# Optimization experiments

Hardware: AMD Instinct MI355X
Metric: run time of the kernel (lower is better)

The kernel has to match this reference:

```python
import jax, jax.numpy as jnp
import numpy as np

B, L, D = 4, 8192, 256          # batch, seq length, embedding dim
H, HD = 8, 32                   # heads, head dim (H*HD == D)
WN, P, S = 9, 4, 1              # window size, padding, stride
EPS = 1e-5


def _layer_norm(x, g, b):
    m = jnp.mean(x, axis=-1, keepdims=True)
    v = jnp.mean(jnp.square(x - m), axis=-1, keepdims=True)
    return (x - m) / jnp.sqrt(v + EPS) * g + b


def setup_inputs() -> dict:
    key = jax.random.key(0)
    ks = jax.random.split(key, 8)
    sc = 0.05
    return {
        "x": jax.random.normal(ks[0], (B, L, D), jnp.float32),
        "W_q": jax.random.normal(ks[1], (D, D), jnp.float32) * sc,
        "W_k": jax.random.normal(ks[2], (D, D), jnp.float32) * sc,
        "W_v": jax.random.normal(ks[3], (D, D), jnp.float32) * sc,
        "W_o": jax.random.normal(ks[4], (D, D), jnp.float32) * sc,
        "pos": jax.random.normal(ks[5], (WN, D), jnp.float32) * sc,
        "W_out": jax.random.normal(ks[6], (D, D), jnp.float32) * sc,
        "b_out": jnp.zeros((D,), jnp.float32),
        "g1": jnp.ones((D,), jnp.float32),
        "b1": jnp.zeros((D,), jnp.float32),
        "g2": jnp.ones((D,), jnp.float32),
        "b2": jnp.zeros((D,), jnp.float32),
    }


def reference(x, W_q, W_k, W_v, W_o, pos, W_out, b_out, g1, b1, g2, b2):
    # input_dim == embedding_dim -> no input projection
    padded = jnp.pad(x, ((0, 0), (P, P), (0, 0)))
    nw = (L + 2 * P - WN) // S + 1  # == L for S=1, WN=2P+1
    idx = jnp.arange(nw)[:, None] * S + jnp.arange(WN)[None, :]  # [nw, WN]
    win = padded[:, idx] + pos  # [B, nw, WN, D]

    def proj(w):  # [B, nw, WN, H, HD]
        return jnp.einsum('bnwd,de->bnwe', win, w).reshape(B, nw, WN, H, HD)

    q, k, v = proj(W_q), proj(W_k), proj(W_v)
    scale = 1.0 / (HD ** 0.5)
    scores = jnp.einsum('bnqhd,bnkhd->bnhqk', q, k) * scale  # [B,nw,H,WN,WN]
    attn = jax.nn.softmax(scores, axis=-1)
    # context, summed over query positions within each window (use_mean=False)
    ctx = jnp.einsum('bnhqk,bnkhd->bnhd', attn, v).reshape(B, nw, D)
    skip = x[:, ::S]  # [B, nw, D]
    attn_res = _layer_norm(skip + ctx @ W_o, g1, b1)
    out = _layer_norm(attn_res @ W_out.T + b_out + attn_res, g2, b2)
    return jax.nn.relu(out)
```

## Files before the change

### kernel.cpp

```cpp
#include <hip/hip_runtime.h>
#include <hip/hip_bf16.h>
#include <math.h>

constexpr int NB   = 4;
constexpr int LL   = 8192;
constexpr int DD   = 256;
constexpr int NH   = 8;
constexpr int HDIM = 32;
constexpr int WNN  = 9;
constexpr int PPAD = 4;

constexpr int CW  = 32;
constexpr int RSN = CW + 8;
constexpr int SST = 260;

typedef __attribute__((ext_vector_type(8))) short bf16x8;
typedef __attribute__((ext_vector_type(4))) float f32x4;

__device__ inline short f2bf(float f) {
  __hip_bfloat16 h = __float2bfloat16(f);
  short s; __builtin_memcpy(&s, &h, 2); return s;
}
__device__ inline float bf2f(short s) {
  unsigned u = ((unsigned)(unsigned short)s) << 16;
  float f; __builtin_memcpy(&f, &u, 4); return f;
}

__global__ __launch_bounds__(256) void conv_x(const float* __restrict__ x, short* __restrict__ XB) {
  size_t i = ((size_t)blockIdx.x * 256 + threadIdx.x) * 4;
  float4 v = *(const float4*)(x + i);
  short4 o; o.x = f2bf(v.x); o.y = f2bf(v.y); o.z = f2bf(v.z); o.w = f2bf(v.w);
  *(short4*)(XB + i) = o;
}

__global__ __launch_bounds__(256) void prep_w(
    const float* __restrict__ Wq, const float* __restrict__ Wk, const float* __restrict__ Wv,
    const float* __restrict__ Wo, const float* __restrict__ Wout,
    short* __restrict__ WqT, short* __restrict__ WkT, short* __restrict__ WvT,
    short* __restrict__ WoT, short* __restrict__ WoutB) {
  const int t = threadIdx.x, b = blockIdx.x;
  if (b < 4) {
    const float* W = (b == 0) ? Wq : (b == 1) ? Wk : (b == 2) ? Wv : Wo;
    short* T = (b == 0) ? WqT : (b == 1) ? WkT : (b == 2) ? WvT : WoT;
    for (int k = 0; k < 256; k += 4) {
      short4 o;
      o.x = f2bf(W[(size_t)(k + 0) * 256 + t]);
      o.y = f2bf(W[(size_t)(k + 1) * 256 + t]);
      o.z = f2bf(W[(size_t)(k + 2) * 256 + t]);
      o.w = f2bf(W[(size_t)(k + 3) * 256 + t]);
      *(short4*)&T[(size_t)t * 256 + k] = o;
    }
  } else {
    for (int i = t; i < 16384; i += 256) {
      float4 v = *(const float4*)(Wout + (size_t)i * 4);
      short4 o; o.x = f2bf(v.x); o.y = f2bf(v.y); o.z = f2bf(v.z); o.w = f2bf(v.w);
      *(short4*)(WoutB + (size_t)i * 4) = o;
    }
  }
}

__global__ __launch_bounds__(256) void pos_proj(
    const float* __restrict__ pos,
    const float* __restrict__ Wq, const float* __restrict__ Wk, const float* __restrict__ Wv,
    short* __restrict__ PQb, short* __restrict__ PKb, short* __restrict__ PVb) {
  __shared__ float ps[256];
  const int t = threadIdx.x, wrow = blockIdx.x, wh = blockIdx.y;
  const float* W = (wh == 0) ? Wq : (wh == 1) ? Wk : Wv;
  short* P = (wh == 0) ? PQb : (wh == 1) ? PKb : PVb;
  ps[t] = pos[wrow * 256 + t];
  __syncthreads();
  float a = 0.f;
  for (int d = 0; d < 256; ++d) a += ps[d] * W[(size_t)d * 256 + t];
  P[wrow * 256 + t] = f2bf(a);
}

__global__ __launch_bounds__(256) void qkv_mfma(
    const short* __restrict__ XB,
    const short* __restrict__ WT0, const short* __restrict__ WT1, const short* __restrict__ WT2,
    short* __restrict__ O0, short* __restrict__ O1, short* __restrict__ O2) {
  const int t = threadIdx.x, w = t >> 6, lane = t & 63, q = lane >> 4, m = lane & 15;
  const size_t row0 = (size_t)blockIdx.x * 64;
  const short* WT = (blockIdx.y == 0) ? WT0 : (blockIdx.y == 1) ? WT1 : WT2;
  short* O = (blockIdx.y == 0) ? O0 : (blockIdx.y == 1) ? O1 : O2;

  f32x4 acc[4][4];
#pragma unroll
  for (int i = 0; i < 4; ++i)
#pragma unroll
    for (int j = 0; j < 4; ++j) acc[i][j] = (f32x4){0.f, 0.f, 0.f, 0.f};

  const short* abase = XB + (row0 + m) * (size_t)256 + q * 8;
  const short* bbase = WT + (size_t)(w * 64 + m) * 256 + q * 8;
  bf16x8 a[4], b[4];
#pragma unroll
  for (int i = 0; i < 4; ++i) a[i] = *(const bf16x8*)(abase + (size_t)i * 4096);
#pragma unroll
  for (int j = 0; j < 4; ++j) b[j] = *(const bf16x8*)(bbase + (size_t)j * 4096);
#pragma unroll
  for (int kk = 0; kk < 8; ++kk) {
    bf16x8 an[4], bn[4];
    if (kk < 7) {
#pragma unroll
      for (int i = 0; i < 4; ++i) an[i] = *(const bf16x8*)(abase + (size_t)i * 4096 + (kk + 1) * 32);
#pragma unroll
      for (int j = 0; j < 4; ++j) bn[j] = *(const bf16x8*)(bbase + (size_t)j * 4096 + (kk + 1) * 32);
    }
#pragma unroll
    for (int i = 0; i < 4; ++i)
#pragma unroll
      for (int j = 0; j < 4; ++j)
        acc[i][j] = __builtin_amdgcn_mfma_f32_16x16x32_bf16(a[i], b[j], acc[i][j], 0, 0, 0);
    if (kk < 7) {
#pragma unroll
      for (int i = 0; i < 4; ++i) a[i] = an[i];
#pragma unroll
      for (int j = 0; j < 4; ++j) b[j] = bn[j];
    }
  }
#pragma unroll
  for (int i = 0; i < 4; ++i)
#pragma unroll
    for (int j = 0; j < 4; ++j)
#pragma unroll
      for (int r = 0; r < 4; ++r) {
        size_t row = row0 + i * 16 + q * 4 + r;
        int col = w * 64 + j * 16 + m;
        O[row * 256 + col] = f2bf(acc[i][j][r]);
      }
}

__global__ __launch_bounds__(256, 2) void attn_kernel(
    const short* __restrict__ XQb, const short* __restrict__ XKb, const short* __restrict__ XVb,
    const short* __restrict__ PQb, const short* __restrict__ PKb, const short* __restrict__ PVb,
    short* __restrict__ CTXB) {
  __shared__ short sq[RSN * SST];
  __shared__ short sk[RSN * SST];
  __shared__ short sv[RSN * SST];
  __shared__ short pq[WNN * SST];
  __shared__ short pk[WNN * SST];
  __shared__ short pv[WNN * SST];

  const int t = threadIdx.x;
  const int nblk = LL / CW;
  const int b = blockIdx.x / nblk;
  const int n0 = (blockIdx.x % nblk) * CW;
  const size_t base = (size_t)b * LL * DD;

  const int lq   = t & 63;
  const int gcol = ((((lq & 7) << 3) | (lq >> 3))) * 4;
  const int pcol = ((lq >> 3) << 5) | ((lq & 7) << 2);

#pragma unroll
  for (int i = 0; i < RSN / 4; ++i) {
    int r = (t >> 6) + i * 4;
    int j = n0 - PPAD + r;
    short4 vq = {0, 0, 0, 0}, vk = vq, vv = vq;
    if (j >= 0 && j < LL) {
      size_t off = base + (size_t)j * DD + gcol;
      vq = *(const short4*)(XQb + off);
      vk = *(const short4*)(XKb + off);
      vv = *(const short4*)(XVb + off);
    }
    *(short4*)&sq[r * SST + pcol] = vq;
    *(short4*)&sk[r * SST + pcol] = vk;
    *(short4*)&sv[r * SST + pcol] = vv;
  }
#pragma unroll
  for (int i = 0; i < 3; ++i) {
    int r = (t >> 6) + i * 4;
    if (r < WNN) {
      *(short4*)&pq[r * SST + pcol] = *(const short4*)(PQb + r * DD + gcol);
      *(short4*)&pk[r * SST + pcol] = *(const short4*)(PKb + r * DD + gcol);
      *(short4*)&pv[r * SST + pcol] = *(const short4*)(PVb + r * DD + gcol);
    }
  }
  __syncthreads();

  const int n = t >> 3;
  const int h = t & 7;
  const int hoff = h * HDIM;
  const int hph = h * 4;

  float sc[WNN][WNN];
#pragma unroll
  for (int qi = 0; qi < WNN; ++qi)
#pragma unroll
    for (int ki = 0; ki < WNN; ++ki) sc[qi][ki] = 0.f;

#pragma unroll
  for (int c = 0; c < 8; ++c) {
    const int cph = c * 32 + hph;
    float qv[WNN][4], kv[WNN][4];
#pragma unroll
    for (int r = 0; r < WNN; ++r) {
      short4 xa = *(const short4*)&sq[(n + r) * SST + cph];
      short4 pa = *(const short4*)&pq[r * SST + cph];
      qv[r][0] = bf2f(xa.x) + bf2f(pa.x);
      qv[r][1] = bf2f(xa.y) + bf2f(pa.y);
      qv[r][2] = bf2f(xa.z) + bf2f(pa.z);
      qv[r][3] = bf2f(xa.w) + bf2f(pa.w);
      short4 xb = *(const short4*)&sk[(n + r) * SST + cph];
      short4 pb = *(const short4*)&pk[r * SST + cph];
      kv[r][0] = bf2f(xb.x) + bf2f(pb.x);
      kv[r][1] = bf2f(xb.y) + bf2f(pb.y);
      kv[r][2] = bf2f(xb.z) + bf2f(pb.z);
      kv[r][3] = bf2f(xb.w) + bf2f(pb.w);
    }
#pragma unroll
    for (int qi = 0; qi < WNN; ++qi)
#pragma unroll
      for (int ki = 0; ki < WNN; ++ki)
        sc[qi][ki] += qv[qi][0] * kv[ki][0] + qv[qi][1] * kv[ki][1] +
                      qv[qi][2] * kv[ki][2] + qv[qi][3] * kv[ki][3];
  }

  float cs[WNN];
#pragma unroll
  for (int ki = 0; ki < WNN; ++ki) cs[ki] = 0.f;
  const float scale = 0.17677669529663687f;
#pragma unroll
  for (int qi = 0; qi < WNN; ++qi) {
    float mx = sc[qi][0];
#pragma unroll
    for (int ki = 1; ki < WNN; ++ki) mx = fmaxf(mx, sc[qi][ki]);
    float e[WNN], sum = 0.f;
#pragma unroll
    for (int ki = 0; ki < WNN; ++ki) { e[ki] = __expf((sc[qi][ki] - mx) * scale); sum += e[ki]; }
    float inv = 1.f / sum;
#pragma unroll
    for (int ki = 0; ki < WNN; ++ki) cs[ki] += e[ki] * inv;
  }

#pragma unroll
  for (int c = 0; c < 8; ++c) {
    const int cph = c * 32 + hph;
    float o0 = 0.f, o1 = 0.f, o2 = 0.f, o3 = 0.f;
#pragma unroll
    for (int ki = 0; ki < WNN; ++ki) {
      short4 xv4 = *(const short4*)&sv[(n + ki) * SST + cph];
      short4 pv4 = *(const short4*)&pv[ki * SST + cph];
      float wt = cs[ki];
      o0 += wt * (bf2f(xv4.x) + bf2f(pv4.x));
      o1 += wt * (bf2f(xv4.y) + bf2f(pv4.y));
      o2 += wt * (bf2f(xv4.z) + bf2f(pv4.z));
      o3 += wt * (bf2f(xv4.w) + bf2f(pv4.w));
    }
    short4 os; os.x = f2bf(o0); os.y = f2bf(o1); os.z = f2bf(o2); os.w = f2bf(o3);
    *(short4*)(CTXB + base + (size_t)(n0 + n) * DD + hoff + c * 4) = os;
  }
}


__global__ __launch_bounds__(256) void out_mfma(
    const short* __restrict__ CTXB, const float* __restrict__ X,
    const short* __restrict__ WoT, const short* __restrict__ WoutB,
    const float* __restrict__ bo,
    const float* __restrict__ g1, const float* __restrict__ b1,
    const float* __restrict__ g2, const float* __restrict__ b2,
    float* __restrict__ out) {
  __shared__ short ar[64 * 264];
  __shared__ float ws1[64][4], ws2[64][4];
  __shared__ float msh[64], rsh[64];
  __shared__ float g1s[256], b1s[256], g2s[256], b2s[256], bos[256];
  const int t = threadIdx.x, w = t >> 6, lane = t & 63, q = lane >> 4, m = lane & 15;
  const size_t row0 = (size_t)blockIdx.x * 64;
  g1s[t] = g1[t]; b1s[t] = b1[t]; g2s[t] = g2[t]; b2s[t] = b2[t]; bos[t] = bo[t];

  f32x4 acc[4][4];
#pragma unroll
  for (int i = 0; i < 4; ++i)
#pragma unroll
    for (int j = 0; j < 4; ++j) acc[i][j] = (f32x4){0.f, 0.f, 0.f, 0.f};

  const short* abase = CTXB + (row0 + m) * (size_t)256 + q * 8;
  const short* bbase = WoT + (size_t)(w * 64 + m) * 256 + q * 8;
  {
    bf16x8 a[4], b[4];
#pragma unroll
    for (int i = 0; i < 4; ++i) a[i] = *(const bf16x8*)(abase + (size_t)i * 4096);
#pragma unroll
    for (int j = 0; j < 4; ++j) b[j] = *(const bf16x8*)(bbase + (size_t)j * 4096);
#pragma unroll
    for (int kk = 0; kk < 8; ++kk) {
      bf16x8 an[4], bn[4];
      if (kk < 7) {
#pragma unroll
        for (int i = 0; i < 4; ++i) an[i] = *(const bf16x8*)(abase + (size_t)i * 4096 + (kk + 1) * 32);
#pragma unroll
        for (int j = 0; j < 4; ++j) bn[j] = *(const bf16x8*)(bbase + (size_t)j * 4096 + (kk + 1) * 32);
      }
#pragma unroll
      for (int i = 0; i < 4; ++i)
#pragma unroll
        for (int j = 0; j < 4; ++j)
          acc[i][j] = __builtin_amdgcn_mfma_f32_16x16x32_bf16(a[i], b[j], acc[i][j], 0, 0, 0);
      if (kk < 7) {
#pragma unroll
        for (int i = 0; i < 4; ++i) a[i] = an[i];
#pragma unroll
        for (int j = 0; j < 4; ++j) b[j] = bn[j];
      }
    }
  }

  float s1v[4][4], s2v[4][4];
#pragma unroll
  for (int i = 0; i < 4; ++i)
#pragma unroll
    for (int r = 0; r < 4; ++r) {
      float a0 = 0.f, b0 = 0.f;
#pragma unroll
      for (int j = 0; j < 4; ++j) {
        float v = acc[i][j][r] + X[(row0 + i * 16 + q * 4 + r) * 256 + w * 64 + j * 16 + m];
        acc[i][j][r] = v; a0 += v; b0 += v * v;
      }
      s1v[i][r] = a0; s2v[i][r] = b0;
    }
#pragma unroll
  for (int i = 0; i < 4; ++i)
#pragma unroll
    for (int r = 0; r < 4; ++r)
#pragma unroll
      for (int msk = 1; msk < 16; msk <<= 1) {
        s1v[i][r] += __shfl_xor(s1v[i][r], msk, 64);
        s2v[i][r] += __shfl_xor(s2v[i][r], msk, 64);
      }
  if (m == 0) {
#pragma unroll
    for (int i = 0; i < 4; ++i)
#pragma unroll
      for (int r = 0; r < 4; ++r) {
        ws1[i * 16 + q * 4 + r][w] = s1v[i][r];
        ws2[i * 16 + q * 4 + r][w] = s2v[i][r];
      }
  }
  __syncthreads();
  if (t < 64) {
    float a0 = 0.f, b0 = 0.f;
#pragma unroll
    for (int ww = 0; ww < 4; ++ww) { a0 += ws1[t][ww]; b0 += ws2[t][ww]; }
    float mean = a0 * (1.f / 256.f);
    float var = b0 * (1.f / 256.f) - mean * mean;
    msh[t] = mean; rsh[t] = rsqrtf(var + 1e-5f);
  }
  __syncthreads();

#pragma unroll
  for (int i = 0; i < 4; ++i)
#pragma unroll
    for (int r = 0; r < 4; ++r) {
      int row = i * 16 + q * 4 + r;
      float mean = msh[row], rst = rsh[row];
#pragma unroll
      for (int j = 0; j < 4; ++j) {
        int col = w * 64 + j * 16 + m;
        float v = (acc[i][j][r] - mean) * rst * g1s[col] + b1s[col];
        ar[row * 264 + col] = f2bf(v);
      }
    }
  __syncthreads();

#pragma unroll
  for (int i = 0; i < 4; ++i)
#pragma unroll
    for (int j = 0; j < 4; ++j) acc[i][j] = (f32x4){0.f, 0.f, 0.f, 0.f};
  const short* b2base = WoutB + (size_t)(w * 64 + m) * 256 + q * 8;
  {
    bf16x8 b[4];
#pragma unroll
    for (int j = 0; j < 4; ++j) b[j] = *(const bf16x8*)(b2base + (size_t)j * 4096);
#pragma unroll
    for (int kk = 0; kk < 8; ++kk) {
      bf16x8 bn[4];
      if (kk < 7) {
#pragma unroll
        for (int j = 0; j < 4; ++j) bn[j] = *(const bf16x8*)(b2base + (size_t)j * 4096 + (kk + 1) * 32);
      }
      bf16x8 a[4];
#pragma unroll
      for (int i = 0; i < 4; ++i) a[i] = *(const bf16x8*)&ar[(i * 16 + m) * 264 + kk * 32 + q * 8];
#pragma unroll
      for (int i = 0; i < 4; ++i)
#pragma unroll
        for (int j = 0; j < 4; ++j)
          acc[i][j] = __builtin_amdgcn_mfma_f32_16x16x32_bf16(a[i], b[j], acc[i][j], 0, 0, 0);
      if (kk < 7) {
#pragma unroll
        for (int j = 0; j < 4; ++j) b[j] = bn[j];
      }
    }
  }

#pragma unroll
  for (int i = 0; i < 4; ++i)
#pragma unroll
    for (int r = 0; r < 4; ++r) {
      int row = i * 16 + q * 4 + r;
      float a0 = 0.f, b0 = 0.f;
#pragma unroll
      for (int j = 0; j < 4; ++j) {
        int col = w * 64 + j * 16 + m;
        float v = acc[i][j][r] + bos[col] + bf2f(ar[row * 264 + col]);
        acc[i][j][r] = v; a0 += v; b0 += v * v;
      }
      s1v[i][r] = a0; s2v[i][r] = b0;
    }
#pragma unroll
  for (int i = 0; i < 4; ++i)
#pragma unroll
    for (int r = 0; r < 4; ++r)
#pragma unroll
      for (int msk = 1; msk < 16; msk <<= 1) {
        s1v[i][r] += __shfl_xor(s1v[i][r], msk, 64);
        s2v[i][r] += __shfl_xor(s2v[i][r], msk, 64);
      }
  if (m == 0) {
#pragma unroll
    for (int i = 0; i < 4; ++i)
#pragma unroll
      for (int r = 0; r < 4; ++r) {
        ws1[i * 16 + q * 4 + r][w] = s1v[i][r];
        ws2[i * 16 + q * 4 + r][w] = s2v[i][r];
      }
  }
  __syncthreads();
  if (t < 64) {
    float a0 = 0.f, b0 = 0.f;
#pragma unroll
    for (int ww = 0; ww < 4; ++ww) { a0 += ws1[t][ww]; b0 += ws2[t][ww]; }
    float mean = a0 * (1.f / 256.f);
    float var = b0 * (1.f / 256.f) - mean * mean;
    msh[t] = mean; rsh[t] = rsqrtf(var + 1e-5f);
  }
  __syncthreads();

#pragma unroll
  for (int i = 0; i < 4; ++i)
#pragma unroll
    for (int r = 0; r < 4; ++r) {
      int row = i * 16 + q * 4 + r;
      float mean = msh[row], rst = rsh[row];
#pragma unroll
      for (int j = 0; j < 4; ++j) {
        int col = w * 64 + j * 16 + m;
        float v = (acc[i][j][r] - mean) * rst * g2s[col] + b2s[col];
        out[(row0 + row) * 256 + col] = fmaxf(v, 0.f);
      }
    }
}

extern "C" void kernel_launch(void* const* d_in, const int* in_sizes, int n_in,
                              void* d_out, int out_size, void* d_ws, size_t ws_size,
                              hipStream_t stream) {
  const float* x    = (const float*)d_in[0];
  const float* Wq   = (const float*)d_in[1];
  const float* Wk   = (const float*)d_in[2];
  const float* Wv   = (const float*)d_in[3];
  const float* Wo   = (const float*)d_in[4];
  const float* pos  = (const float*)d_in[5];
  const float* Wout = (const float*)d_in[6];
  const float* bo   = (const float*)d_in[7];
  const float* g1   = (const float*)d_in[8];
  const float* b1   = (const float*)d_in[9];
  const float* g2   = (const float*)d_in[10];
  const float* b2   = (const float*)d_in[11];
  float* out = (float*)d_out;

  const size_t nel = (size_t)NB * LL * DD;
  char* wsb = (char*)d_ws;
  short* XB   = (short*)wsb; wsb += nel * 2;
  short* XQb  = (short*)wsb; wsb += nel * 2;
  short* XKb  = (short*)wsb; wsb += nel * 2;
  short* XVb  = (short*)wsb; wsb += nel * 2;
  short* CTXB = (short*)wsb; wsb += nel * 2;
  short* WqT   = (short*)wsb; wsb += 65536 * 2;
  short* WkT   = (short*)wsb; wsb += 65536 * 2;
  short* WvT   = (short*)wsb; wsb += 65536 * 2;
  short* WoT   = (short*)wsb; wsb += 65536 * 2;
  short* WoutB = (short*)wsb; wsb += 65536 * 2;
  short* PQb = (short*)wsb; wsb += WNN * DD * 2;
  short* PKb = (short*)wsb; wsb += WNN * DD * 2;
  short* PVb = (short*)wsb; wsb += WNN * DD * 2;

  conv_x<<<(unsigned)(nel / 4 / 256), 256, 0, stream>>>(x, XB);
  prep_w<<<5, 256, 0, stream>>>(Wq, Wk, Wv, Wo, Wout, WqT, WkT, WvT, WoT, WoutB);
  pos_proj<<<dim3(WNN, 3), 256, 0, stream>>>(pos, Wq, Wk, Wv, PQb, PKb, PVb);
  qkv_mfma<<<dim3((unsigned)(NB * LL / 64), 3), 256, 0, stream>>>(XB, WqT, WkT, WvT, XQb, XKb, XVb);
  attn_kernel<<<NB * (LL / CW), 256, 0, stream>>>(XQb, XKb, XVb, PQb, PKb, PVb, CTXB);
  out_mfma<<<(unsigned)(NB * LL / 64), 256, 0, stream>>>(CTXB, x, WoT, WoutB, bo, g1, b1, g2, b2, out);
}
```

Before: 266.5 us.

## Reuse Q shared buffer for V to cut LDS and raise attention occupancy

The attention kernel now holds V rows and V positional rows in registers during the score phase. After the softmax it writes them into the shared buffer that held Q, so only two row buffers and two position buffers stay resident instead of three of each. The column permutation is changed so stores are contiguous, and the position-row stride drops its padding. Launch bounds rise to three blocks per SM to use the freed LDS. The cost is an extra barrier pair and more register pressure from the prefetched V values, which may limit the higher occupancy.

```diff
diff --git a/kernel.cpp b/kernel.cpp
--- a/kernel.cpp
+++ b/kernel.cpp
@@ -13,6 +13,7 @@
 constexpr int CW  = 32;
 constexpr int RSN = CW + 8;
 constexpr int SST = 260;
+constexpr int PST = 256;
 
 typedef __attribute__((ext_vector_type(8))) short bf16x8;
 typedef __attribute__((ext_vector_type(4))) float f32x4;
@@ -129,16 +130,14 @@
       }
 }
 
-__global__ __launch_bounds__(256, 2) void attn_kernel(
+__global__ __launch_bounds__(256, 3) void attn_kernel(
     const short* __restrict__ XQb, const short* __restrict__ XKb, const short* __restrict__ XVb,
     const short* __restrict__ PQb, const short* __restrict__ PKb, const short* __restrict__ PVb,
     short* __restrict__ CTXB) {
-  __shared__ short sq[RSN * SST];
-  __shared__ short sk[RSN * SST];
-  __shared__ short sv[RSN * SST];
-  __shared__ short pq[WNN * SST];
-  __shared__ short pk[WNN * SST];
-  __shared__ short pv[WNN * SST];
+  __shared__ short sA[RSN * SST];
+  __shared__ short sK[RSN * SST];
+  __shared__ short pA[WNN * PST];
+  __shared__ short pK[WNN * PST];
 
   const int t = threadIdx.x;
   const int nblk = LL / CW;
@@ -147,31 +146,46 @@
   const size_t base = (size_t)b * LL * DD;
 
   const int lq   = t & 63;
-  const int gcol = ((((lq & 7) << 3) | (lq >> 3))) * 4;
-  const int pcol = ((lq >> 3) << 5) | ((lq & 7) << 2);
-
+  const int sh_h = (lq & 31) >> 2;
+  const int sh_c = (lq & 3) | ((lq >> 5) << 2);
+  const int gcol = (sh_h * 8 + sh_c) * 4;
+  const int pcol = lq * 4;
+
+  short4 vreg[RSN / 4];
 #pragma unroll
   for (int i = 0; i < RSN / 4; ++i) {
     int r = (t >> 6) + i * 4;
     int j = n0 - PPAD + r;
-    short4 vq = {0, 0, 0, 0}, vk = vq, vv = vq;
+    short4 vv = {0, 0, 0, 0};
+    if (j >= 0 && j < LL) vv = *(const short4*)(XVb + base + (size_t)j * DD + gcol);
+    vreg[i] = vv;
+  }
+  short4 pvreg[3];
+#pragma unroll
+  for (int i = 0; i < 3; ++i) {
+    int r = (t >> 6) + i * 4;
+    pvreg[i] = (r < WNN) ? *(const short4*)(PVb + r * DD + gcol) : (short4){0, 0, 0, 0};
+  }
+
+#pragma unroll
+  for (int i = 0; i < RSN / 4; ++i) {
+    int r = (t >> 6) + i * 4;
+    int j = n0 - PPAD + r;
+    short4 vq = {0, 0, 0, 0}, vk = vq;
     if (j >= 0 && j < LL) {
       size_t off = base + (size_t)j * DD + gcol;
       vq = *(const short4*)(XQb + off);
       vk = *(const short4*)(XKb + off);
-      vv = *(const short4*)(XVb + off);
-    }
-    *(short4*)&sq[r * SST + pcol] = vq;
-    *(short4*)&sk[r * SST + pcol] = vk;
-    *(short4*)&sv[r * SST + pcol] = vv;
+    }
+    *(short4*)&sA[r * SST + pcol] = vq;
+    *(short4*)&sK[r * SST + pcol] = vk;
   }
 #pragma unroll
   for (int i = 0; i < 3; ++i) {
     int r = (t >> 6) + i * 4;
     if (r < WNN) {
-      *(short4*)&pq[r * SST + pcol] = *(const short4*)(PQb + r * DD + gcol);
-      *(short4*)&pk[r * SST + pcol] = *(const short4*)(PKb + r * DD + gcol);
-      *(short4*)&pv[r * SST + pcol] = *(const short4*)(PVb + r * DD + gcol);
+      *(short4*)&pA[r * PST + pcol] = *(const short4*)(PQb + r * DD + gcol);
+      *(short4*)&pK[r * PST + pcol] = *(const short4*)(PKb + r * DD + gcol);
     }
   }
   __syncthreads();
@@ -179,7 +193,6 @@
   const int n = t >> 3;
   const int h = t & 7;
   const int hoff = h * HDIM;
-  const int hph = h * 4;
 
   float sc[WNN][WNN];
 #pragma unroll
@@ -189,18 +202,18 @@
 
 #pragma unroll
   for (int c = 0; c < 8; ++c) {
-    const int cph = c * 32 + hph;
+    const int cph = h * 16 + (c & 3) * 4 + (c >> 2) * 128;
     float qv[WNN][4], kv[WNN][4];
 #pragma unroll
     for (int r = 0; r < WNN; ++r) {
-      short4 xa = *(const short4*)&sq[(n + r) * SST + cph];
-      short4 pa = *(const short4*)&pq[r * SST + cph];
+      short4 xa = *(const short4*)&sA[(n + r) * SST + cph];
+      short4 pa = *(const short4*)&pA[r * PST + cph];
       qv[r][0] = bf2f(xa.x) + bf2f(pa.x);
       qv[r][1] = bf2f(xa.y) + bf2f(pa.y);
       qv[r][2] = bf2f(xa.z) + bf2f(pa.z);
       qv[r][3] = bf2f(xa.w) + bf2f(pa.w);
-      short4 xb = *(const short4*)&sk[(n + r) * SST + cph];
-      short4 pb = *(const short4*)&pk[r * SST + cph];
+      short4 xb = *(const short4*)&sK[(n + r) * SST + cph];
+      short4 pb = *(const short4*)&pK[r * PST + cph];
       kv[r][0] = bf2f(xb.x) + bf2f(pb.x);
       kv[r][1] = bf2f(xb.y) + bf2f(pb.y);
       kv[r][2] = bf2f(xb.z) + bf2f(pb.z);
@@ -231,14 +244,27 @@
     for (int ki = 0; ki < WNN; ++ki) cs[ki] += e[ki] * inv;
   }
 
+  __syncthreads();
+#pragma unroll
+  for (int i = 0; i < RSN / 4; ++i) {
+    int r = (t >> 6) + i * 4;
+    *(short4*)&sA[r * SST + pcol] = vreg[i];
+  }
+#pragma unroll
+  for (int i = 0; i < 3; ++i) {
+    int r = (t >> 6) + i * 4;
+    if (r < WNN) *(short4*)&pA[r * PST + pcol] = pvreg[i];
+  }
+  __syncthreads();
+
 #pragma unroll
   for (int c = 0; c < 8; ++c) {
-    const int cph = c * 32 + hph;
+    const int cph = h * 16 + (c & 3) * 4 + (c >> 2) * 128;
     float o0 = 0.f, o1 = 0.f, o2 = 0.f, o3 = 0.f;
 #pragma unroll
     for (int ki = 0; ki < WNN; ++ki) {
-      short4 xv4 = *(const short4*)&sv[(n + ki) * SST + cph];
-      short4 pv4 = *(const short4*)&pv[ki * SST + cph];
+      short4 xv4 = *(const short4*)&sA[(n + ki) * SST + cph];
+      short4 pv4 = *(const short4*)&pA[ki * PST + cph];
       float wt = cs[ki];
       o0 += wt * (bf2f(xv4.x) + bf2f(pv4.x));
       o1 += wt * (bf2f(xv4.y) + bf2f(pv4.y));
```

Result: slower. 711.0 us (+166.8%).
